# Kernel optimization log

Measured on AMD Instinct MI355X. Metric: run time of the kernel, lower is better.

## Reference

```python
import jax, jax.numpy as jnp
import numpy as np


def setup_inputs() -> dict:
    key = jax.random.key(0)
    ks = jax.random.split(key, 7)
    B, Nc, Nt = 4, 2048, 2048
    D = 512          # key_size == representation_size
    H, E = 8, 64     # num_heads, head_dim = D // H
    return {
        "keys": jax.random.normal(ks[0], (B, Nc, D), dtype=jnp.float32),
        "values": jax.random.normal(ks[1], (B, Nc, D), dtype=jnp.float32),
        "query": jax.random.normal(ks[2], (B, Nt, D), dtype=jnp.float32),
        "Wk": jax.random.normal(ks[3], (H, D, E), dtype=jnp.float32) * 0.02,
        "Wv": jax.random.normal(ks[4], (H, D, E), dtype=jnp.float32) * 0.02,
        "Wq": jax.random.normal(ks[5], (H, D, E), dtype=jnp.float32) * 0.02,
        "Wout": jax.random.normal(ks[6], (D, D), dtype=jnp.float32) * 0.02,
    }


def reference(keys, values, query, Wk, Wv, Wq, Wout):
    # Batched per-head projections (replaces the per-head Python loop)
    k = jnp.einsum("bnd,hde->bhne", keys, Wk)    # [B,H,Nc,E]
    v = jnp.einsum("bnd,hde->bhne", values, Wv)  # [B,H,Nc,E]
    q = jnp.einsum("bnd,hde->bhne", query, Wq)   # [B,H,Nt,E]
    head_dim = q.shape[-1]
    # NOTE: original scales by head_dim (query.size()[2]), not sqrt(head_dim)
    scores = jnp.einsum("bhqe,bhke->bhqk", q, k) / head_dim
    attn = jax.nn.softmax(scores, axis=-1)
    out = jnp.einsum("bhqk,bhke->bhqe", attn, v)  # [B,H,Nt,E]
    # concat over heads (head-major feature order, matches torch.cat(dim=-1))
    B, H, Nt, E = out.shape
    out = jnp.transpose(out, (0, 2, 1, 3)).reshape(B, Nt, H * E)
    # final Linear (no bias): x @ Wout^T
    return out @ Wout.T
```

## Files before the change

### kernel.cpp

```cpp
#include <hip/hip_runtime.h>

#define B_   4
#define H_   8
#define NSEQ 2048
#define D_   512
#define E_   64

typedef __bf16 bf16x8 __attribute__((ext_vector_type(8)));
typedef float  f32x4  __attribute__((ext_vector_type(4)));
typedef float  f32x16 __attribute__((ext_vector_type(16)));

__device__ __forceinline__ unsigned short f2b(float f) {
    __bf16 h = (__bf16)f;
    return __builtin_bit_cast(unsigned short, h);
}
__device__ __forceinline__ unsigned pk2(float a, float b) {
    return (unsigned)f2b(a) | ((unsigned)f2b(b) << 16);
}
__device__ __forceinline__ bf16x8 ld_frag(const unsigned short* p) {
    return *reinterpret_cast<const bf16x8*>(p);
}
__device__ __forceinline__ void async_copy16(const void* g, const unsigned short* l) {
    __builtin_amdgcn_global_load_lds(
        (const __attribute__((address_space(1))) unsigned int*)g,
        (__attribute__((address_space(3))) unsigned int*)l, 16, 0, 0);
}

__device__ __forceinline__ int lds_blk(int r, int s) {
    int lr = r >> 1;
    return lr * 128 + (((((r & 1) << 3) | s) ^ (lr & 15)) << 3);
}
#define STAGE_SRC(r0, l, row, slot)                                            \
    {   int lr_ = ((r0) >> 1) + ((l) >> 4);                                    \
        int B_x = ((l) & 15) ^ (lr_ & 15);                                     \
        row = (lr_ << 1) | (B_x >> 3);  slot = B_x & 7; }

__global__ __launch_bounds__(256)
void cast_w_kernel(const float* __restrict__ Wk, const float* __restrict__ Wv,
                   const float* __restrict__ Wq, const float* __restrict__ Wo,
                   unsigned short* __restrict__ okt, unsigned short* __restrict__ ovt,
                   unsigned short* __restrict__ oqt, unsigned short* __restrict__ oo) {
    int idx = blockIdx.x * 256 + threadIdx.x;
    int y = blockIdx.y;
    if (y == 3) { oo[idx] = f2b(Wo[idx]); return; }
    const float* src = y == 0 ? Wk : (y == 1 ? Wv : Wq);
    unsigned short* dst = y == 0 ? okt : (y == 1 ? ovt : oqt);
    float scl = (y == 2) ? 0.015625f : 1.0f;
    int hh = idx >> 15, rem = idx & 32767, d = rem >> 6, e = rem & 63;
    dst[hh * 32768 + e * 512 + d] = f2b(src[idx] * scl);
}

__global__ __launch_bounds__(256)
void xcast_kernel(const float* __restrict__ q, const float* __restrict__ k,
                  const float* __restrict__ v,
                  unsigned short* __restrict__ qx, unsigned short* __restrict__ kx,
                  unsigned short* __restrict__ vx) {
    const int y = blockIdx.y;
    const float* src = y == 0 ? q : (y == 1 ? k : v);
    unsigned short* dst = y == 0 ? qx : (y == 1 ? kx : vx);
    #pragma unroll
    for (int i = 0; i < 4; ++i) {
        int e = blockIdx.x * 4096 + i * 1024 + threadIdx.x * 4;
        float4 f = *reinterpret_cast<const float4*>(src + e);
        *reinterpret_cast<ushort4*>(dst + e) =
            make_ushort4(f2b(f.x), f2b(f.y), f2b(f.z), f2b(f.w));
    }
}

__global__ __launch_bounds__(256, 3)
void proj_gemm(const unsigned short* __restrict__ qx,
               const unsigned short* __restrict__ kx,
               const unsigned short* __restrict__ vx,
               const unsigned short* __restrict__ wqt,
               const unsigned short* __restrict__ wkt,
               const unsigned short* __restrict__ wvt,
               unsigned short* __restrict__ qb, unsigned short* __restrict__ kb,
               unsigned short* __restrict__ vtb) {
    const int m0  = blockIdx.x * 128;
    const int no0 = blockIdx.y * 64;
    const int which = blockIdx.z;
    const int tid = threadIdx.x;
    const int wave = tid >> 6, lane = tid & 63;
    const int quad = lane >> 4, l16 = lane & 15;

    const unsigned short* X = which == 0 ? qx : (which == 1 ? kx : vx);
    const unsigned short* W = which == 0 ? wqt : (which == 1 ? wkt : wvt);

    __shared__ unsigned short Ab[2][8192];
    __shared__ unsigned short Bb[2][4096];

    const unsigned short* Xp = X + (size_t)m0 * D_;
    const unsigned short* Wp = W + (size_t)no0 * D_;

    int rowA[4], slA[4], rowB[2], slB[2];
    #pragma unroll
    for (int i = 0; i < 4; ++i) STAGE_SRC(wave * 32 + i * 8, lane, rowA[i], slA[i])
    #pragma unroll
    for (int i = 0; i < 2; ++i) STAGE_SRC(wave * 16 + i * 8, lane, rowB[i], slB[i])

    #define PROJ_STAGE(kt, buf)                                                \
        {   _Pragma("unroll")                                                  \
            for (int i = 0; i < 4; ++i)                                        \
                async_copy16(Xp + (size_t)rowA[i] * D_ + (kt) * 64 + slA[i] * 8, \
                             &Ab[buf][(wave * 32 + i * 8) * 64]);              \
            _Pragma("unroll")                                                  \
            for (int i = 0; i < 2; ++i)                                        \
                async_copy16(Wp + (size_t)rowB[i] * D_ + (kt) * 64 + slB[i] * 8, \
                             &Bb[buf][(wave * 16 + i * 8) * 64]);              \
        }

    PROJ_STAGE(0, 0)
    __syncthreads();

    const f32x4 z = {0.f, 0.f, 0.f, 0.f};
    f32x4 acc[2][4];
    #pragma unroll
    for (int i = 0; i < 2; ++i)
        #pragma unroll
        for (int j = 0; j < 4; ++j) acc[i][j] = z;

    for (int kt = 0; kt < 8; ++kt) {
        const int cur = kt & 1;
        if (kt + 1 < 8) PROJ_STAGE(kt + 1, 1 - cur)
        #pragma unroll
        for (int kk = 0; kk < 2; ++kk) {
            const int s = kk * 4 + quad;
            bf16x8 bfr[4];
            #pragma unroll
            for (int nt = 0; nt < 4; ++nt)
                bfr[nt] = ld_frag(&Bb[cur][lds_blk(nt * 16 + l16, s)]);
            #pragma unroll
            for (int mt = 0; mt < 2; ++mt) {
                bf16x8 af = ld_frag(&Ab[cur][lds_blk(wave * 32 + mt * 16 + l16, s)]);
                #pragma unroll
                for (int nt = 0; nt < 4; ++nt)
                    acc[mt][nt] = __builtin_amdgcn_mfma_f32_16x16x32_bf16(
                        af, bfr[nt], acc[mt][nt], 0, 0, 0);
            }
        }
        __syncthreads();
    }

    if (which != 2) {
        unsigned short (*Os)[72] = reinterpret_cast<unsigned short(*)[72]>(&Ab[0][0]);
        #pragma unroll
        for (int mt = 0; mt < 2; ++mt)
            #pragma unroll
            for (int nt = 0; nt < 4; ++nt)
                #pragma unroll
                for (int r = 0; r < 4; ++r)
                    Os[wave * 32 + mt * 16 + quad * 4 + r][nt * 16 + l16] =
                        f2b(acc[mt][nt][r]);
        __syncthreads();
        unsigned short* Y = (which == 0 ? qb : kb);
        #pragma unroll
        for (int i = 0; i < 4; ++i) {
            int idx = tid + i * 256;
            int row = idx >> 3, seg = idx & 7;
            *reinterpret_cast<uint4*>(Y + (size_t)(m0 + row) * D_ + no0 + seg * 8) =
                *reinterpret_cast<const uint4*>(&Os[row][seg * 8]);
        }
    } else {
        unsigned short (*Ot)[136] = reinterpret_cast<unsigned short(*)[136]>(&Ab[0][0]);
        #pragma unroll
        for (int mt = 0; mt < 2; ++mt)
            #pragma unroll
            for (int nt = 0; nt < 4; ++nt) {
                ushort4 o = make_ushort4(f2b(acc[mt][nt][0]), f2b(acc[mt][nt][1]),
                                         f2b(acc[mt][nt][2]), f2b(acc[mt][nt][3]));
                *reinterpret_cast<ushort4*>(
                    &Ot[nt * 16 + l16][wave * 32 + mt * 16 + quad * 4]) = o;
            }
        __syncthreads();
        const int b = m0 >> 11, nloc = m0 & 2047;
        #pragma unroll
        for (int i = 0; i < 4; ++i) {
            int idx = tid + i * 256;
            int lhe = idx >> 4, seg = idx & 15;
            int ghe = no0 + lhe;
            *reinterpret_cast<uint4*>(
                vtb + ((size_t)(b * H_ + (ghe >> 6)) * E_ + (ghe & 63)) * NSEQ +
                nloc + seg * 8) =
                *reinterpret_cast<const uint4*>(&Ot[lhe][seg * 8]);
        }
    }
    #undef PROJ_STAGE
}

__global__ __launch_bounds__(256, 3)
void attn_kernel(const unsigned short* __restrict__ qbp,
                 const unsigned short* __restrict__ kbp,
                 const unsigned short* __restrict__ vtbp,
                 unsigned short* __restrict__ aob) {
    const int L = blockIdx.x;
    const int bh = L & 31, qt = L >> 5;
    const int b = bh >> 3, h = bh & 7;
    const int n0 = qt * 64;
    const int tid = threadIdx.x;
    const int wave = tid >> 6, lane = tid & 63;
    const int wk = wave >> 1, wq = wave & 1;
    const int l32 = lane & 31, hi = lane >> 5;

    __shared__ unsigned short Ks[2][4096];
    __shared__ unsigned short Vs[2][4096];

    const unsigned short* kbase = kbp + (size_t)(b * NSEQ) * D_ + h * 64;
    const unsigned short* vbase = vtbp + (size_t)(b * H_ + h) * E_ * NSEQ;

    int rowS[2], slS[2];
    #pragma unroll
    for (int i = 0; i < 2; ++i) STAGE_SRC(wave * 16 + i * 8, lane, rowS[i], slS[i])

    bf16x8 qf[4];
    #pragma unroll
    for (int ks = 0; ks < 4; ++ks)
        qf[ks] = ld_frag(qbp + (size_t)(b * NSEQ + n0 + wq * 32 + l32) * D_ +
                         h * 64 + ks * 16 + hi * 8);

    #define ATTN_STAGE(j, buf)                                                 \
        {   _Pragma("unroll")                                                  \
            for (int i = 0; i < 2; ++i) {                                      \
                async_copy16(                                                  \
                    kbase + (size_t)((j) * 64 + rowS[i]) * D_ + slS[i] * 8,    \
                    &Ks[buf][wave * 1024 + i * 512]);                          \
                async_copy16(                                                  \
                    vbase + (size_t)rowS[i] * NSEQ + (j) * 64 + slS[i] * 8,    \
                    &Vs[buf][wave * 1024 + i * 512]);                          \
            } }

    ATTN_STAGE(0, 0)
    __syncthreads();

    f32x16 oacc[2] = {};
    float lacc = 0.f;

    for (int j = 0; j < NSEQ / 64; ++j) {
        const int cur = j & 1;
        if (j + 1 < NSEQ / 64) ATTN_STAGE(j + 1, 1 - cur)

        const unsigned short* Kc = Ks[cur];
        const unsigned short* Vc = Vs[cur];

        f32x16 sacc = {};
        #pragma unroll
        for (int ks = 0; ks < 4; ++ks) {
            bf16x8 kf = ld_frag(&Kc[lds_blk(wk * 32 + l32, ks * 2 + hi)]);
            sacc = __builtin_amdgcn_mfma_f32_32x32x16_bf16(kf, qf[ks], sacc, 0, 0, 0);
        }

        float p[16];
        #pragma unroll
        for (int r = 0; r < 16; ++r) p[r] = __expf(sacc[r]);
        lacc += ((p[0] + p[1]) + (p[2] + p[3])) + ((p[4] + p[5]) + (p[6] + p[7])) +
                (((p[8] + p[9]) + (p[10] + p[11])) + ((p[12] + p[13]) + (p[14] + p[15])));

        #pragma unroll
        for (int s = 0; s < 2; ++s) {
            unsigned x0 = pk2(p[s * 8 + 0], p[s * 8 + 1]);
            unsigned x1 = pk2(p[s * 8 + 2], p[s * 8 + 3]);
            unsigned y0 = pk2(p[s * 8 + 4], p[s * 8 + 5]);
            unsigned y1 = pk2(p[s * 8 + 6], p[s * 8 + 7]);
            asm volatile("v_permlane32_swap_b32 %0, %1" : "+v"(x0), "+v"(y0));
            asm volatile("v_permlane32_swap_b32 %0, %1" : "+v"(x1), "+v"(y1));
            uint4 u = make_uint4(x0, x1, y0, y1);
            bf16x8 pb = __builtin_bit_cast(bf16x8, u);
            #pragma unroll
            for (int eb = 0; eb < 2; ++eb) {
                bf16x8 vf = ld_frag(&Vc[lds_blk(eb * 32 + l32, wk * 4 + s * 2 + hi)]);
                oacc[eb] = __builtin_amdgcn_mfma_f32_32x32x16_bf16(
                    vf, pb, oacc[eb], 0, 0, 0);
            }
        }

        __syncthreads();
    }

    lacc += __shfl_xor(lacc, 32);
    float* Of = reinterpret_cast<float*>(&Ks[0][0]);
    float* Lf = reinterpret_cast<float*>(&Vs[0][0]);
    if (wk == 0) {
        #pragma unroll
        for (int eb = 0; eb < 2; ++eb)
            #pragma unroll
            for (int rg = 0; rg < 4; ++rg) {
                f32x4 v = {oacc[eb][rg * 4 + 0], oacc[eb][rg * 4 + 1],
                           oacc[eb][rg * 4 + 2], oacc[eb][rg * 4 + 3]};
                *reinterpret_cast<f32x4*>(
                    &Of[(wq * 32 + l32) * 64 + eb * 32 + rg * 8 + hi * 4]) = v;
            }
        if (hi == 0) Lf[wq * 32 + l32] = lacc;
    }
    __syncthreads();
    if (wk == 1) {
        const float li = 1.0f / (lacc + Lf[wq * 32 + l32]);
        unsigned short* op =
            aob + (size_t)(b * NSEQ + n0 + wq * 32 + l32) * D_ + h * 64;
        #pragma unroll
        for (int eb = 0; eb < 2; ++eb)
            #pragma unroll
            for (int rg = 0; rg < 4; ++rg) {
                const f32x4 o = *reinterpret_cast<const f32x4*>(
                    &Of[(wq * 32 + l32) * 64 + eb * 32 + rg * 8 + hi * 4]);
                ushort4 st = make_ushort4(f2b((oacc[eb][rg * 4 + 0] + o.x) * li),
                                          f2b((oacc[eb][rg * 4 + 1] + o.y) * li),
                                          f2b((oacc[eb][rg * 4 + 2] + o.z) * li),
                                          f2b((oacc[eb][rg * 4 + 3] + o.w) * li));
                *reinterpret_cast<ushort4*>(op + eb * 32 + rg * 8 + hi * 4) = st;
            }
    }
    #undef ATTN_STAGE
}

__global__ __launch_bounds__(256, 3)
void out_gemm(const unsigned short* __restrict__ A,
              const unsigned short* __restrict__ Wo,
              float* __restrict__ Out) {
    const int m0  = blockIdx.x * 128;
    const int no0 = blockIdx.y * 64;
    const int tid = threadIdx.x;
    const int wave = tid >> 6, lane = tid & 63;
    const int quad = lane >> 4, l16 = lane & 15;

    __shared__ unsigned short Ab[2][8192];
    __shared__ unsigned short Bb[2][4096];

    const unsigned short* Ap = A + (size_t)m0 * D_;
    const unsigned short* Bp = Wo + (size_t)no0 * D_;

    int rowA[4], slA[4], rowB[2], slB[2];
    #pragma unroll
    for (int i = 0; i < 4; ++i) STAGE_SRC(wave * 32 + i * 8, lane, rowA[i], slA[i])
    #pragma unroll
    for (int i = 0; i < 2; ++i) STAGE_SRC(wave * 16 + i * 8, lane, rowB[i], slB[i])

    #define OUT_STAGE(kt, buf)                                                 \
        {   _Pragma("unroll")                                                  \
            for (int i = 0; i < 4; ++i)                                        \
                async_copy16(Ap + (size_t)rowA[i] * D_ + (kt) * 64 + slA[i] * 8, \
                             &Ab[buf][(wave * 32 + i * 8) * 64]);              \
            _Pragma("unroll")                                                  \
            for (int i = 0; i < 2; ++i)                                        \
                async_copy16(Bp + (size_t)rowB[i] * D_ + (kt) * 64 + slB[i] * 8, \
                             &Bb[buf][(wave * 16 + i * 8) * 64]);              \
        }

    OUT_STAGE(0, 0)
    __syncthreads();

    const f32x4 z = {0.f, 0.f, 0.f, 0.f};
    f32x4 acc[2][4];
    #pragma unroll
    for (int i = 0; i < 2; ++i)
        #pragma unroll
        for (int j = 0; j < 4; ++j) acc[i][j] = z;

    for (int kt = 0; kt < 8; ++kt) {
        const int cur = kt & 1;
        if (kt + 1 < 8) OUT_STAGE(kt + 1, 1 - cur)
        #pragma unroll
        for (int kk = 0; kk < 2; ++kk) {
            const int s = kk * 4 + quad;
            bf16x8 bfr[4];
            #pragma unroll
            for (int nt = 0; nt < 4; ++nt)
                bfr[nt] = ld_frag(&Bb[cur][lds_blk(nt * 16 + l16, s)]);
            #pragma unroll
            for (int mt = 0; mt < 2; ++mt) {
                bf16x8 af = ld_frag(&Ab[cur][lds_blk(wave * 32 + mt * 16 + l16, s)]);
                #pragma unroll
                for (int nt = 0; nt < 4; ++nt)
                    acc[mt][nt] = __builtin_amdgcn_mfma_f32_16x16x32_bf16(
                        af, bfr[nt], acc[mt][nt], 0, 0, 0);
            }
        }
        __syncthreads();
    }
    #pragma unroll
    for (int mt = 0; mt < 2; ++mt)
        #pragma unroll
        for (int nt = 0; nt < 4; ++nt)
            #pragma unroll
            for (int r = 0; r < 4; ++r)
                Out[(size_t)(m0 + wave * 32 + mt * 16 + quad * 4 + r) * D_ +
                    no0 + nt * 16 + l16] = acc[mt][nt][r];
    #undef OUT_STAGE
}

extern "C" void kernel_launch(void* const* d_in, const int* in_sizes, int n_in,
                              void* d_out, int out_size, void* d_ws, size_t ws_size,
                              hipStream_t stream) {
    const float* keys   = (const float*)d_in[0];
    const float* values = (const float*)d_in[1];
    const float* query  = (const float*)d_in[2];
    const float* Wk     = (const float*)d_in[3];
    const float* Wv     = (const float*)d_in[4];
    const float* Wq     = (const float*)d_in[5];
    const float* Wout   = (const float*)d_in[6];
    float* out = (float*)d_out;

    unsigned short* ws16 = (unsigned short*)d_ws;
    const size_t XN = (size_t)B_ * NSEQ * D_;
    const size_t WN = (size_t)H_ * D_ * E_;
    unsigned short* wkt = ws16;
    unsigned short* wvt = wkt + WN;
    unsigned short* wqt = wvt + WN;
    unsigned short* wob = wqt + WN;
    unsigned short* qb  = wob + WN;
    unsigned short* kb  = qb + XN;
    unsigned short* vtb = kb + XN;
    unsigned short* aob = vtb + XN;
    unsigned short* qx  = aob + XN;
    unsigned short* kx  = qx + XN;
    unsigned short* vx  = aob;

    cast_w_kernel<<<dim3(1024, 4), 256, 0, stream>>>(Wk, Wv, Wq, Wout,
                                                     wkt, wvt, wqt, wob);

    xcast_kernel<<<dim3(1024, 3), 256, 0, stream>>>(query, keys, values,
                                                    qx, kx, vx);

    proj_gemm<<<dim3(64, 8, 3), 256, 0, stream>>>(
        qx, kx, vx, wqt, wkt, wvt, qb, kb, vtb);

    attn_kernel<<<dim3(1024), 256, 0, stream>>>(qb, kb, vtb, aob);

    out_gemm<<<dim3(64, 8), 256, 0, stream>>>(aob, wob, out);
}
```

Measured before the change: 190.2 us.

## Split attention KV across all four waves with 128-key tiles and cross-wave reduction

```diff
diff --git a/kernel.cpp b/kernel.cpp
--- a/kernel.cpp
+++ b/kernel.cpp
@@ -34,6 +34,9 @@
     {   int lr_ = ((r0) >> 1) + ((l) >> 4);                                    \
         int B_x = ((l) & 15) ^ (lr_ & 15);                                     \
         row = (lr_ << 1) | (B_x >> 3);  slot = B_x & 7; }
+__device__ __forceinline__ int lds_blkV(int r, int s) {
+    return r * 128 + ((s ^ (r & 15)) << 3);
+}
 
 __global__ __launch_bounds__(256)
 void cast_w_kernel(const float* __restrict__ Wk, const float* __restrict__ Wv,
@@ -187,7 +190,7 @@
     #undef PROJ_STAGE
 }
 
-__global__ __launch_bounds__(256, 3)
+__global__ __launch_bounds__(256, 2)
 void attn_kernel(const unsigned short* __restrict__ qbp,
                  const unsigned short* __restrict__ kbp,
                  const unsigned short* __restrict__ vtbp,
@@ -198,115 +201,145 @@
     const int n0 = qt * 64;
     const int tid = threadIdx.x;
     const int wave = tid >> 6, lane = tid & 63;
-    const int wk = wave >> 1, wq = wave & 1;
     const int l32 = lane & 31, hi = lane >> 5;
 
-    __shared__ unsigned short Ks[2][4096];
-    __shared__ unsigned short Vs[2][4096];
+    __shared__ unsigned short SM[34304];
+    unsigned short* Ksm = SM;
+    unsigned short* Vsm = SM + 16384;
+    float* Op = reinterpret_cast<float*>(SM);
+    float* Ls = reinterpret_cast<float*>(SM + 33792);
 
     const unsigned short* kbase = kbp + (size_t)(b * NSEQ) * D_ + h * 64;
     const unsigned short* vbase = vtbp + (size_t)(b * H_ + h) * E_ * NSEQ;
 
-    int rowS[2], slS[2];
-    #pragma unroll
-    for (int i = 0; i < 2; ++i) STAGE_SRC(wave * 16 + i * 8, lane, rowS[i], slS[i])
-
-    bf16x8 qf[4];
-    #pragma unroll
-    for (int ks = 0; ks < 4; ++ks)
-        qf[ks] = ld_frag(qbp + (size_t)(b * NSEQ + n0 + wq * 32 + l32) * D_ +
-                         h * 64 + ks * 16 + hi * 8);
+    int rowK[4], slK[4];
+    #pragma unroll
+    for (int i = 0; i < 4; ++i) STAGE_SRC(wave * 32 + i * 8, lane, rowK[i], slK[i])
+    int rowV[4], slV[4];
+    #pragma unroll
+    for (int i = 0; i < 4; ++i) {
+        int r = wave * 16 + i * 4 + (lane >> 4);
+        rowV[i] = r; slV[i] = (lane & 15) ^ (r & 15);
+    }
+
+    bf16x8 qf[2][4];
+    #pragma unroll
+    for (int qh = 0; qh < 2; ++qh)
+        #pragma unroll
+        for (int ks = 0; ks < 4; ++ks)
+            qf[qh][ks] = ld_frag(
+                qbp + (size_t)(b * NSEQ + n0 + qh * 32 + l32) * D_ +
+                h * 64 + ks * 16 + hi * 8);
 
     #define ATTN_STAGE(j, buf)                                                 \
         {   _Pragma("unroll")                                                  \
-            for (int i = 0; i < 2; ++i) {                                      \
+            for (int i = 0; i < 4; ++i) {                                      \
                 async_copy16(                                                  \
-                    kbase + (size_t)((j) * 64 + rowS[i]) * D_ + slS[i] * 8,    \
-                    &Ks[buf][wave * 1024 + i * 512]);                          \
+                    kbase + (size_t)((j) * 128 + rowK[i]) * D_ + slK[i] * 8,   \
+                    Ksm + (buf) * 8192 + (wave * 32 + i * 8) * 64);            \
                 async_copy16(                                                  \
-                    vbase + (size_t)rowS[i] * NSEQ + (j) * 64 + slS[i] * 8,    \
-                    &Vs[buf][wave * 1024 + i * 512]);                          \
+                    vbase + (size_t)rowV[i] * NSEQ + (j) * 128 + slV[i] * 8,   \
+                    Vsm + (buf) * 8192 + (wave * 16 + i * 4) * 128);           \
             } }
 
     ATTN_STAGE(0, 0)
     __syncthreads();
 
-    f32x16 oacc[2] = {};
-    float lacc = 0.f;
-
-    for (int j = 0; j < NSEQ / 64; ++j) {
+    f32x16 oacc[2][2] = {};
+    float lacc0 = 0.f, lacc1 = 0.f;
+
+    for (int j = 0; j < NSEQ / 128; ++j) {
         const int cur = j & 1;
-        if (j + 1 < NSEQ / 64) ATTN_STAGE(j + 1, 1 - cur)
-
-        const unsigned short* Kc = Ks[cur];
-        const unsigned short* Vc = Vs[cur];
-
-        f32x16 sacc = {};
+        if (j + 1 < NSEQ / 128) ATTN_STAGE(j + 1, 1 - cur)
+
+        const unsigned short* Kc = Ksm + cur * 8192;
+        const unsigned short* Vc = Vsm + cur * 8192;
+
+        f32x16 s0 = {}, s1 = {};
         #pragma unroll
         for (int ks = 0; ks < 4; ++ks) {
-            bf16x8 kf = ld_frag(&Kc[lds_blk(wk * 32 + l32, ks * 2 + hi)]);
-            sacc = __builtin_amdgcn_mfma_f32_32x32x16_bf16(kf, qf[ks], sacc, 0, 0, 0);
-        }
-
-        float p[16];
-        #pragma unroll
-        for (int r = 0; r < 16; ++r) p[r] = __expf(sacc[r]);
-        lacc += ((p[0] + p[1]) + (p[2] + p[3])) + ((p[4] + p[5]) + (p[6] + p[7])) +
-                (((p[8] + p[9]) + (p[10] + p[11])) + ((p[12] + p[13]) + (p[14] + p[15])));
+            bf16x8 kf = ld_frag(&Kc[lds_blk(wave * 32 + l32, ks * 2 + hi)]);
+            s0 = __builtin_amdgcn_mfma_f32_32x32x16_bf16(kf, qf[0][ks], s0, 0, 0, 0);
+            s1 = __builtin_amdgcn_mfma_f32_32x32x16_bf16(kf, qf[1][ks], s1, 0, 0, 0);
+        }
+
+        float p0[16], p1[16];
+        float ls0 = 0.f, ls1 = 0.f;
+        #pragma unroll
+        for (int r = 0; r < 16; ++r) { p0[r] = __expf(s0[r]); ls0 += p0[r]; }
+        #pragma unroll
+        for (int r = 0; r < 16; ++r) { p1[r] = __expf(s1[r]); ls1 += p1[r]; }
+        lacc0 += ls0; lacc1 += ls1;
 
         #pragma unroll
         for (int s = 0; s < 2; ++s) {
-            unsigned x0 = pk2(p[s * 8 + 0], p[s * 8 + 1]);
-            unsigned x1 = pk2(p[s * 8 + 2], p[s * 8 + 3]);
-            unsigned y0 = pk2(p[s * 8 + 4], p[s * 8 + 5]);
-            unsigned y1 = pk2(p[s * 8 + 6], p[s * 8 + 7]);
-            asm volatile("v_permlane32_swap_b32 %0, %1" : "+v"(x0), "+v"(y0));
-            asm volatile("v_permlane32_swap_b32 %0, %1" : "+v"(x1), "+v"(y1));
-            uint4 u = make_uint4(x0, x1, y0, y1);
-            bf16x8 pb = __builtin_bit_cast(bf16x8, u);
+            unsigned a0 = pk2(p0[s * 8 + 0], p0[s * 8 + 1]);
+            unsigned a1 = pk2(p0[s * 8 + 2], p0[s * 8 + 3]);
+            unsigned b0 = pk2(p0[s * 8 + 4], p0[s * 8 + 5]);
+            unsigned b1 = pk2(p0[s * 8 + 6], p0[s * 8 + 7]);
+            asm volatile("v_permlane32_swap_b32 %0, %1" : "+v"(a0), "+v"(b0));
+            asm volatile("v_permlane32_swap_b32 %0, %1" : "+v"(a1), "+v"(b1));
+            uint4 u0 = make_uint4(a0, a1, b0, b1);
+            bf16x8 pb0 = __builtin_bit_cast(bf16x8, u0);
+            unsigned c0 = pk2(p1[s * 8 + 0], p1[s * 8 + 1]);
+            unsigned c1 = pk2(p1[s * 8 + 2], p1[s * 8 + 3]);
+            unsigned d0 = pk2(p1[s * 8 + 4], p1[s * 8 + 5]);
+            unsigned d1 = pk2(p1[s * 8 + 6], p1[s * 8 + 7]);
+            asm volatile("v_permlane32_swap_b32 %0, %1" : "+v"(c0), "+v"(d0));
+            asm volatile("v_permlane32_swap_b32 %0, %1" : "+v"(c1), "+v"(d1));
+            uint4 u1 = make_uint4(c0, c1, d0, d1);
+            bf16x8 pb1 = __builtin_bit_cast(bf16x8, u1);
             #pragma unroll
             for (int eb = 0; eb < 2; ++eb) {
-                bf16x8 vf = ld_frag(&Vc[lds_blk(eb * 32 + l32, wk * 4 + s * 2 + hi)]);
-                oacc[eb] = __builtin_amdgcn_mfma_f32_32x32x16_bf16(
-                    vf, pb, oacc[eb], 0, 0, 0);
+                bf16x8 vf = ld_frag(
+                    &Vc[lds_blkV(eb * 32 + l32, wave * 4 + s * 2 + hi)]);
+                oacc[0][eb] = __builtin_amdgcn_mfma_f32_32x32x16_bf16(
+                    vf, pb0, oacc[0][eb], 0, 0, 0);
+                oacc[1][eb] = __builtin_amdgcn_mfma_f32_32x32x16_bf16(
+                    vf, pb1, oacc[1][eb], 0, 0, 0);
             }
         }
 
         __syncthreads();
     }
 
-    lacc += __shfl_xor(lacc, 32);
-    float* Of = reinterpret_cast<float*>(&Ks[0][0]);
-    float* Lf = reinterpret_cast<float*>(&Vs[0][0]);
-    if (wk == 0) {
+    lacc0 += __shfl_xor(lacc0, 32);
+    lacc1 += __shfl_xor(lacc1, 32);
+    #pragma unroll
+    for (int qh = 0; qh < 2; ++qh)
         #pragma unroll
         for (int eb = 0; eb < 2; ++eb)
             #pragma unroll
             for (int rg = 0; rg < 4; ++rg) {
-                f32x4 v = {oacc[eb][rg * 4 + 0], oacc[eb][rg * 4 + 1],
-                           oacc[eb][rg * 4 + 2], oacc[eb][rg * 4 + 3]};
+                f32x4 v = {oacc[qh][eb][rg * 4 + 0], oacc[qh][eb][rg * 4 + 1],
+                           oacc[qh][eb][rg * 4 + 2], oacc[qh][eb][rg * 4 + 3]};
                 *reinterpret_cast<f32x4*>(
-                    &Of[(wq * 32 + l32) * 64 + eb * 32 + rg * 8 + hi * 4]) = v;
+                    &Op[wave * 4224 + (qh * 32 + l32) * 66 +
+                        eb * 32 + rg * 8 + hi * 4]) = v;
             }
-        if (hi == 0) Lf[wq * 32 + l32] = lacc;
+    if (hi == 0) {
+        Ls[wave * 64 + l32]      = lacc0;
+        Ls[wave * 64 + 32 + l32] = lacc1;
     }
     __syncthreads();
-    if (wk == 1) {
-        const float li = 1.0f / (lacc + Lf[wq * 32 + l32]);
+    {
+        const int q  = wave * 16 + (lane >> 2);
+        const int ec = (lane & 3) * 16;
+        const float li = 1.0f / (Ls[q] + Ls[64 + q] + Ls[128 + q] + Ls[192 + q]);
         unsigned short* op =
-            aob + (size_t)(b * NSEQ + n0 + wq * 32 + l32) * D_ + h * 64;
-        #pragma unroll
-        for (int eb = 0; eb < 2; ++eb)
-            #pragma unroll
-            for (int rg = 0; rg < 4; ++rg) {
-                const f32x4 o = *reinterpret_cast<const f32x4*>(
-                    &Of[(wq * 32 + l32) * 64 + eb * 32 + rg * 8 + hi * 4]);
-                ushort4 st = make_ushort4(f2b((oacc[eb][rg * 4 + 0] + o.x) * li),
-                                          f2b((oacc[eb][rg * 4 + 1] + o.y) * li),
-                                          f2b((oacc[eb][rg * 4 + 2] + o.z) * li),
-                                          f2b((oacc[eb][rg * 4 + 3] + o.w) * li));
-                *reinterpret_cast<ushort4*>(op + eb * 32 + rg * 8 + hi * 4) = st;
-            }
+            aob + (size_t)(b * NSEQ + n0 + q) * D_ + h * 64 + ec;
+        #pragma unroll
+        for (int i = 0; i < 4; ++i) {
+            const int e = ec + i * 4;
+            f32x4 a = *reinterpret_cast<const f32x4*>(&Op[q * 66 + e]);
+            f32x4 a1 = *reinterpret_cast<const f32x4*>(&Op[4224 + q * 66 + e]);
+            f32x4 a2 = *reinterpret_cast<const f32x4*>(&Op[8448 + q * 66 + e]);
+            f32x4 a3 = *reinterpret_cast<const f32x4*>(&Op[12672 + q * 66 + e]);
+            a = (a + a1) + (a2 + a3);
+            ushort4 st = make_ushort4(f2b(a.x * li), f2b(a.y * li),
+                                      f2b(a.z * li), f2b(a.w * li));
+            *reinterpret_cast<ushort4*>(op + i * 4) = st;
+        }
     }
     #undef ATTN_STAGE
 }
```

Result: slower. 200.5 us (+5.4%).
